# Performance work log

Measured on AMD Instinct MI355X. Metric: run time of the kernel, lower is better.

Reference implementation:

```python
import jax, jax.numpy as jnp
import numpy as np

B, S, D, H, F = 4, 2048, 1024, 16, 4096
DK = D // H
EPS = 1e-5


def layer_norm(x, gamma, beta):
    mu = jnp.mean(x, axis=-1, keepdims=True)
    var = jnp.mean(jnp.square(x - mu), axis=-1, keepdims=True)
    return (x - mu) * jax.lax.rsqrt(var + EPS) * gamma + beta


def setup_inputs() -> dict:
    key = jax.random.key(0)
    ks = jax.random.split(key, 16)
    s = 1.0 / np.sqrt(D)
    sf = 1.0 / np.sqrt(F)
    inp = {
        "x": jax.random.normal(ks[0], (B, S, D), dtype=jnp.float32),
        # causal mask: 0 = blocked, 1 = visible (masked_fill(mask == 0, -1e9))
        "mask": jnp.tril(jnp.ones((S, S), dtype=jnp.int32))[None, None],
        "Wq": jax.random.normal(ks[1], (D, D), dtype=jnp.float32) * s,
        "bq": jnp.zeros((D,), dtype=jnp.float32),
        "Wk": jax.random.normal(ks[2], (D, D), dtype=jnp.float32) * s,
        "bk": jnp.zeros((D,), dtype=jnp.float32),
        "Wv": jax.random.normal(ks[3], (D, D), dtype=jnp.float32) * s,
        "bv": jnp.zeros((D,), dtype=jnp.float32),
        "Wo": jax.random.normal(ks[4], (D, D), dtype=jnp.float32) * s,
        "bo": jnp.zeros((D,), dtype=jnp.float32),
        "g1": jnp.ones((D,), dtype=jnp.float32),
        "b1": jnp.zeros((D,), dtype=jnp.float32),
        "W1": jax.random.normal(ks[5], (D, F), dtype=jnp.float32) * s,
        "c1": jnp.zeros((F,), dtype=jnp.float32),
        "W2": jax.random.normal(ks[6], (F, D), dtype=jnp.float32) * sf,
        "c2": jnp.zeros((D,), dtype=jnp.float32),
        "g2": jnp.ones((D,), dtype=jnp.float32),
        "b2": jnp.zeros((D,), dtype=jnp.float32),
    }
    return inp


def reference(x, mask, Wq, bq, Wk, bk, Wv, bv, Wo, bo, g1, b1, W1, c1, W2, c2, g2, b2):
    b = x.shape[0]
    # qkv projections -> [B, H, S, DK]
    q = (x @ Wq + bq).reshape(b, S, H, DK).transpose(0, 2, 1, 3)
    k = (x @ Wk + bk).reshape(b, S, H, DK).transpose(0, 2, 1, 3)
    v = (x @ Wv + bv).reshape(b, S, H, DK).transpose(0, 2, 1, 3)
    scores = jnp.einsum("bhqd,bhkd->bhqk", q, k) / np.sqrt(DK)
    scores = jnp.where(mask == 0, -1e9, scores)
    attn = jax.nn.softmax(scores, axis=-1)
    out = jnp.einsum("bhqk,bhkd->bhqd", attn, v)
    out = out.transpose(0, 2, 1, 3).reshape(b, S, D)
    attended = out @ Wo + bo
    x = layer_norm(x + attended, g1, b1)
    ff = jax.nn.relu(x @ W1 + c1) @ W2 + c2
    x = layer_norm(x + ff, g2, b2)
    return x
```

## Files before the change

kernel.cpp:

```cpp
#include <hip/hip_runtime.h>
#include <cstdint>
#include <cstddef>

#define DEV __device__ __forceinline__

typedef unsigned short u16;
typedef __attribute__((ext_vector_type(8))) short bf16x8;
typedef __attribute__((ext_vector_type(8))) u16  u16x8;
typedef __attribute__((ext_vector_type(4))) float f32x4;

constexpr int Bn = 4, Sn = 2048, Dn = 1024, Hn = 16, Fn = 4096, DKn = 64;
constexpr int Mn = Bn * Sn;

DEV u16 f2b(float f) {
    unsigned u = __float_as_uint(f);
    unsigned r = (u + 0x7fffu + ((u >> 16) & 1u)) >> 16;
    return (u16)r;
}
DEV float b2f(u16 h) { return __uint_as_float(((unsigned)h) << 16); }

typedef __attribute__((address_space(1))) void gvoid;
typedef __attribute__((address_space(3))) void lvoid;
DEV void gl_lds16(const u16* g, u16* l) {
    __builtin_amdgcn_global_load_lds((gvoid*)g, (lvoid*)l, 16, 0, 0);
}

DEV f32x4 mfma16(bf16x8 a, bf16x8 b, f32x4 c) {
    return __builtin_amdgcn_mfma_f32_16x16x32_bf16(a, b, c, 0, 0, 0);
}

__global__ __launch_bounds__(256) void cvt_f32_bf16(const float* __restrict__ in,
                                                    u16* __restrict__ out) {
    size_t i = ((size_t)blockIdx.x * 256 + threadIdx.x) * 8;
    float4 a = *(const float4*)(in + i);
    float4 b = *(const float4*)(in + i + 4);
    u16x8 o;
    o[0] = f2b(a.x); o[1] = f2b(a.y); o[2] = f2b(a.z); o[3] = f2b(a.w);
    o[4] = f2b(b.x); o[5] = f2b(b.y); o[6] = f2b(b.z); o[7] = f2b(b.w);
    *(u16x8*)(out + i) = o;
}

__global__ __launch_bounds__(256) void transpose_cvt(const float* __restrict__ W,
                                                     u16* __restrict__ Wt, int K, int N) {
    __shared__ float tile[32][33];
    int n0 = blockIdx.x * 32, k0 = blockIdx.y * 32;
    int tx = threadIdx.x, ty = threadIdx.y;
    for (int r = ty; r < 32; r += 8) tile[r][tx] = W[(size_t)(k0 + r) * N + n0 + tx];
    __syncthreads();
    for (int r = ty; r < 32; r += 8) Wt[(size_t)(n0 + r) * K + k0 + tx] = f2b(tile[tx][r]);
}

__global__ __launch_bounds__(256) void vt_kernel(const u16* __restrict__ V,
                                                 u16* __restrict__ Vt) {
    __shared__ u16 t[32][34];
    int s0 = blockIdx.x * 32, d0 = blockIdx.y * 32, bh = blockIdx.z;
    int tx = threadIdx.x, ty = threadIdx.y;
    const u16* in = V + (size_t)bh * Sn * DKn;
    u16* out = Vt + (size_t)bh * DKn * Sn;
    for (int r = ty; r < 32; r += 8) t[r][tx] = in[(size_t)(s0 + r) * DKn + d0 + tx];
    __syncthreads();
    for (int r = ty; r < 32; r += 8) out[(size_t)(d0 + r) * Sn + s0 + tx] = t[tx][r];
}

template <int RELU, int RESID, int OUT_BF16, int QKV>
__global__ __launch_bounds__(256) void gemm_kernel(
    const u16* __restrict__ A, const u16* __restrict__ Bt,
    const float* __restrict__ bias,
    const float* __restrict__ residF, const u16* __restrict__ residB,
    float* __restrict__ Cf, u16* __restrict__ Cb,
    int M, int N, int K, float oscale) {
    constexpr int BK = 32;
    __shared__ __align__(16) u16 As[128 * BK];
    __shared__ __align__(16) u16 Bs[128 * BK];
    const int tid = threadIdx.x, wave = tid >> 6, lane = tid & 63;
    const int quad = lane >> 4, l16 = lane & 15;
    const int row0 = blockIdx.x * 128, col0 = blockIdx.y * 128;
    const int wm = wave & 1, wn = wave >> 1;

    f32x4 acc[4][4];
    for (int mt = 0; mt < 4; mt++)
        for (int nt = 0; nt < 4; nt++)
            acc[mt][nt] = f32x4{0.f, 0.f, 0.f, 0.f};

    const int srow = lane >> 2, scol = (lane & 3) * 8;
    const u16* Ag = A + (size_t)(row0 + wave * 16 + srow) * K + scol;
    const u16* Bg = Bt + (size_t)(col0 + wave * 16 + srow) * K + scol;
    u16* AsW = As + (wave * 16) * BK;
    u16* BsW = Bs + (wave * 16) * BK;

    for (int k0 = 0; k0 < K; k0 += BK) {
        __syncthreads();
        gl_lds16(Ag + k0, AsW);
        gl_lds16(Ag + (size_t)64 * K + k0, AsW + 64 * BK);
        gl_lds16(Bg + k0, BsW);
        gl_lds16(Bg + (size_t)64 * K + k0, BsW + 64 * BK);
        __syncthreads();

        bf16x8 af[4], bfr[4];
        for (int mt = 0; mt < 4; mt++)
            af[mt] = *(const bf16x8*)(As + (wm * 64 + mt * 16 + l16) * BK + quad * 8);
        for (int nt = 0; nt < 4; nt++)
            bfr[nt] = *(const bf16x8*)(Bs + (wn * 64 + nt * 16 + l16) * BK + quad * 8);
        for (int mt = 0; mt < 4; mt++)
            for (int nt = 0; nt < 4; nt++)
                acc[mt][nt] = mfma16(af[mt], bfr[nt], acc[mt][nt]);
    }

    for (int nt = 0; nt < 4; nt++) {
        int col = col0 + wn * 64 + nt * 16 + l16;
        float bv = bias[col];
        for (int mt = 0; mt < 4; mt++) {
            int rbase = row0 + wm * 64 + mt * 16 + quad * 4;
            for (int r = 0; r < 4; r++) {
                int row = rbase + r;
                float v = acc[mt][nt][r] + bv;
                if (RELU) v = fmaxf(v, 0.f);
                if (RESID == 1) v += residF[(size_t)row * N + col];
                if (RESID == 2) v += b2f(residB[(size_t)row * N + col]);
                if (QKV) {
                    int bb = row >> 11, s = row & 2047, h = col >> 6, dk = col & 63;
                    Cb[((size_t)(bb * Hn + h) * Sn + s) * DKn + dk] = f2b(v * oscale);
                } else if (OUT_BF16) {
                    Cb[(size_t)row * N + col] = f2b(v);
                } else {
                    Cf[(size_t)row * N + col] = v;
                }
            }
        }
    }
}

__global__ __launch_bounds__(256, 4) void attn3_kernel(const u16* __restrict__ Q,
                                                       const u16* __restrict__ K,
                                                       const u16* __restrict__ Vt,
                                                       u16* __restrict__ O) {
    constexpr int STR = 72;
    __shared__ __align__(16) u16 Ks[64 * 64];
    __shared__ __align__(16) u16 Vs[64 * 64];
    __shared__ __align__(16) u16 Ps[4][16 * STR];
    int tid = threadIdx.x, wave = tid >> 6, lane = tid & 63;
    int quad = lane >> 4, l16 = lane & 15;
    int bh = blockIdx.y, b = bh >> 4, h = bh & 15;
    int p = blockIdx.x;
    const u16* Qh = Q + (size_t)bh * Sn * DKn;
    const u16* Kh = K + (size_t)bh * Sn * DKn;
    const u16* Vh = Vt + (size_t)bh * DKn * Sn;
    u16* Pw = &Ps[wave][0];

    const int srow = wave * 16 + (lane >> 3);
    const int sblk = lane & 7;
    u16* KsW = Ks + wave * 16 * 64;
    u16* VsW = Vs + wave * 16 * 64;

    for (int t = 0; t < 2; t++) {
        int qt = t ? p : 31 - p;
        int R0 = qt * 64 + wave * 16;

        bf16x8 qf[2];
        for (int h2 = 0; h2 < 2; h2++)
            qf[h2] = *(const bf16x8*)(Qh + (size_t)(R0 + l16) * DKn + h2 * 32 + quad * 8);

        float m_i[4], l_i[4];
        f32x4 accO[4];
        for (int r = 0; r < 4; r++) { m_i[r] = -1e30f; l_i[r] = 0.f; }
        for (int nt = 0; nt < 4; nt++) accO[nt] = f32x4{0.f, 0.f, 0.f, 0.f};

        for (int kt = 0; kt <= qt; kt++) {
            __syncthreads();
            for (int i = 0; i < 2; i++) {
                int r = srow + i * 8;
                int gb = sblk ^ (r & 7);
                gl_lds16(Kh + (size_t)(kt * 64 + r) * DKn + gb * 8, KsW + i * 512);
                gl_lds16(Vh + (size_t)r * Sn + kt * 64 + gb * 8, VsW + i * 512);
            }
            __syncthreads();

            f32x4 sc[4];
            for (int nt = 0; nt < 4; nt++) sc[nt] = f32x4{0.f, 0.f, 0.f, 0.f};
            for (int h2 = 0; h2 < 2; h2++) {
                int bswz = ((h2 * 4 + quad) ^ (l16 & 7)) * 8;
                for (int nt = 0; nt < 4; nt++) {
                    bf16x8 kf = *(const bf16x8*)(Ks + (nt * 16 + l16) * 64 + bswz);
                    sc[nt] = mfma16(qf[h2], kf, sc[nt]);
                }
            }

            if (kt == qt) {
                for (int r = 0; r < 4; r++)
                    for (int nt = 0; nt < 4; nt++)
                        if (nt * 16 + l16 > wave * 16 + quad * 4 + r) sc[nt][r] = -1e30f;
            }

            for (int r = 0; r < 4; r++) {
                float mx = fmaxf(fmaxf(sc[0][r], sc[1][r]), fmaxf(sc[2][r], sc[3][r]));
                for (int off = 1; off < 16; off <<= 1) mx = fmaxf(mx, __shfl_xor(mx, off, 64));
                float mn = fmaxf(m_i[r], mx);
                float al = exp2f(m_i[r] - mn);
                m_i[r] = mn;
                float ps = 0.f;
                for (int nt = 0; nt < 4; nt++) {
                    float pv = exp2f(sc[nt][r] - mn);
                    sc[nt][r] = pv;
                    ps += pv;
                }
                l_i[r] = l_i[r] * al + ps;
                for (int nt = 0; nt < 4; nt++) accO[nt][r] *= al;
            }

            for (int r = 0; r < 4; r++)
                for (int nt = 0; nt < 4; nt++)
                    Pw[(quad * 4 + r) * STR + nt * 16 + l16] = f2b(sc[nt][r]);
            for (int h2 = 0; h2 < 2; h2++) {
                bf16x8 pf = *(const bf16x8*)(Pw + l16 * STR + h2 * 32 + quad * 8);
                int bswz = ((h2 * 4 + quad) ^ (l16 & 7)) * 8;
                for (int nt = 0; nt < 4; nt++) {
                    bf16x8 vf = *(const bf16x8*)(Vs + (nt * 16 + l16) * 64 + bswz);
                    accO[nt] = mfma16(pf, vf, accO[nt]);
                }
            }
        }

        for (int r = 0; r < 4; r++) {
            float lr = l_i[r];
            for (int off = 1; off < 16; off <<= 1) lr += __shfl_xor(lr, off, 64);
            float inv = 1.f / lr;
            int sg = R0 + quad * 4 + r;
            for (int nt = 0; nt < 4; nt++)
                O[((size_t)b * Sn + sg) * Dn + h * DKn + nt * 16 + l16] = f2b(accO[nt][r] * inv);
        }
    }
}

template <int OUT_BF16>
__global__ __launch_bounds__(256) void ln_kernel(const float* __restrict__ in,
                                                 const float* __restrict__ gamma,
                                                 const float* __restrict__ beta,
                                                 float* __restrict__ outF,
                                                 u16* __restrict__ outB) {
    int row = blockIdx.x, tid = threadIdx.x;
    float4 v = ((const float4*)(in + (size_t)row * Dn))[tid];
    float s = v.x + v.y + v.z + v.w;
    float q = v.x * v.x + v.y * v.y + v.z * v.z + v.w * v.w;
    for (int off = 32; off >= 1; off >>= 1) {
        s += __shfl_xor(s, off, 64);
        q += __shfl_xor(q, off, 64);
    }
    __shared__ float rs[4], rq[4];
    int wave = tid >> 6, lane = tid & 63;
    if (lane == 0) { rs[wave] = s; rq[wave] = q; }
    __syncthreads();
    s = rs[0] + rs[1] + rs[2] + rs[3];
    q = rq[0] + rq[1] + rq[2] + rq[3];
    float mu = s * (1.f / Dn);
    float rstd = rsqrtf(q * (1.f / Dn) - mu * mu + 1e-5f);
    float4 g = ((const float4*)gamma)[tid];
    float4 be = ((const float4*)beta)[tid];
    float o0 = (v.x - mu) * rstd * g.x + be.x;
    float o1 = (v.y - mu) * rstd * g.y + be.y;
    float o2 = (v.z - mu) * rstd * g.z + be.z;
    float o3 = (v.w - mu) * rstd * g.w + be.w;
    if (OUT_BF16) {
        ushort4 u;
        u.x = f2b(o0); u.y = f2b(o1); u.z = f2b(o2); u.w = f2b(o3);
        ((ushort4*)outB)[(size_t)row * (Dn / 4) + tid] = u;
    } else {
        ((float4*)outF)[(size_t)row * (Dn / 4) + tid] = make_float4(o0, o1, o2, o3);
    }
}

extern "C" void kernel_launch(void* const* d_in, const int* in_sizes, int n_in,
                              void* d_out, int out_size, void* d_ws, size_t ws_size,
                              hipStream_t stream) {
    const float* x  = (const float*)d_in[0];
    const float* Wq = (const float*)d_in[2];  const float* bq = (const float*)d_in[3];
    const float* Wk = (const float*)d_in[4];  const float* bk = (const float*)d_in[5];
    const float* Wv = (const float*)d_in[6];  const float* bv = (const float*)d_in[7];
    const float* Wo = (const float*)d_in[8];  const float* bo = (const float*)d_in[9];
    const float* g1 = (const float*)d_in[10]; const float* b1 = (const float*)d_in[11];
    const float* W1 = (const float*)d_in[12]; const float* c1 = (const float*)d_in[13];
    const float* W2 = (const float*)d_in[14]; const float* c2 = (const float*)d_in[15];
    const float* g2 = (const float*)d_in[16]; const float* b2 = (const float*)d_in[17];

    char* ws = (char*)d_ws;
    const size_t MB = 1ull << 20;
    u16*   Xb  = (u16*)(ws + 0 * MB);
    u16*   WqT = (u16*)(ws + 16 * MB);
    u16*   WkT = (u16*)(ws + 18 * MB);
    u16*   WvT = (u16*)(ws + 20 * MB);
    u16*   WoT = (u16*)(ws + 22 * MB);
    u16*   W1T = (u16*)(ws + 24 * MB);
    u16*   W2T = (u16*)(ws + 32 * MB);
    u16*   Qb  = (u16*)(ws + 40 * MB);
    u16*   Kb  = (u16*)(ws + 56 * MB);
    u16*   Vb  = (u16*)(ws + 72 * MB);
    u16*   Ob  = (u16*)(ws + 88 * MB);
    u16*   Vt  = (u16*)(ws + 104 * MB);
    float* h1  = (float*)(ws + 104 * MB);
    u16*   ff1 = (u16*)(ws + 136 * MB);
    u16*   ln1b = Qb;
    float* h2   = h1;

    const float qscale = 0.125f * 1.44269504f;

    dim3 tb(32, 8);
    cvt_f32_bf16<<<dim3(Mn * Dn / (256 * 8)), 256, 0, stream>>>(x, Xb);
    transpose_cvt<<<dim3(Dn / 32, Dn / 32), tb, 0, stream>>>(Wq, WqT, Dn, Dn);
    transpose_cvt<<<dim3(Dn / 32, Dn / 32), tb, 0, stream>>>(Wk, WkT, Dn, Dn);
    transpose_cvt<<<dim3(Dn / 32, Dn / 32), tb, 0, stream>>>(Wv, WvT, Dn, Dn);
    transpose_cvt<<<dim3(Dn / 32, Dn / 32), tb, 0, stream>>>(Wo, WoT, Dn, Dn);
    transpose_cvt<<<dim3(Fn / 32, Dn / 32), tb, 0, stream>>>(W1, W1T, Dn, Fn);
    transpose_cvt<<<dim3(Dn / 32, Fn / 32), tb, 0, stream>>>(W2, W2T, Fn, Dn);

    gemm_kernel<0, 0, 1, 1><<<dim3(Mn / 128, Dn / 128), 256, 0, stream>>>(
        Xb, WqT, bq, nullptr, nullptr, nullptr, Qb, Mn, Dn, Dn, qscale);
    gemm_kernel<0, 0, 1, 1><<<dim3(Mn / 128, Dn / 128), 256, 0, stream>>>(
        Xb, WkT, bk, nullptr, nullptr, nullptr, Kb, Mn, Dn, Dn, 1.0f);
    gemm_kernel<0, 0, 1, 1><<<dim3(Mn / 128, Dn / 128), 256, 0, stream>>>(
        Xb, WvT, bv, nullptr, nullptr, nullptr, Vb, Mn, Dn, Dn, 1.0f);

    vt_kernel<<<dim3(Sn / 32, DKn / 32, Bn * Hn), tb, 0, stream>>>(Vb, Vt);

    attn3_kernel<<<dim3(16, Bn * Hn), 256, 0, stream>>>(Qb, Kb, Vt, Ob);

    gemm_kernel<0, 1, 0, 0><<<dim3(Mn / 128, Dn / 128), 256, 0, stream>>>(
        Ob, WoT, bo, x, nullptr, h1, nullptr, Mn, Dn, Dn, 1.0f);
    ln_kernel<1><<<Mn, 256, 0, stream>>>(h1, g1, b1, nullptr, ln1b);

    gemm_kernel<1, 0, 1, 0><<<dim3(Mn / 128, Fn / 128), 256, 0, stream>>>(
        ln1b, W1T, c1, nullptr, nullptr, nullptr, ff1, Mn, Fn, Dn, 1.0f);
    gemm_kernel<0, 2, 0, 0><<<dim3(Mn / 128, Dn / 128), 256, 0, stream>>>(
        ff1, W2T, c2, nullptr, ln1b, h2, nullptr, Mn, Dn, Fn, 1.0f);
    ln_kernel<0><<<Mn, 256, 0, stream>>>(h2, g2, b2, (float*)d_out, nullptr);
}
```

Baseline: 620.7 us.

## Fuse QKV projections into one GEMM and use 128-key attention tiles

The three Q/K/V projection GEMMs become a single launch over N=3*D. Each column block picks its bias and output scale by group and writes to the matching head-major buffer, which cuts launch count and gives a larger grid. The attention kernel now processes 128 keys per iteration instead of 64 and reuses the K shared buffer for the P tile. That halves the number of load/sync rounds per query tile, but needs an extra barrier and wastes half a tile of masked work on even diagonal tiles. The fused GEMM assumes the transposed Q/K/V weights and the Q/K/V output buffers sit contiguously in the workspace.

```diff
diff --git a/kernel.cpp b/kernel.cpp
--- a/kernel.cpp
+++ b/kernel.cpp
@@ -65,7 +65,8 @@
 template <int RELU, int RESID, int OUT_BF16, int QKV>
 __global__ __launch_bounds__(256) void gemm_kernel(
     const u16* __restrict__ A, const u16* __restrict__ Bt,
-    const float* __restrict__ bias,
+    const float* __restrict__ bias, const float* __restrict__ biasB,
+    const float* __restrict__ biasC,
     const float* __restrict__ residF, const u16* __restrict__ residB,
     float* __restrict__ Cf, u16* __restrict__ Cb,
     int M, int N, int K, float oscale) {
@@ -106,9 +107,17 @@
                 acc[mt][nt] = mfma16(af[mt], bfr[nt], acc[mt][nt]);
     }
 
+    int g = 0; const float* bp = bias; float osc = 1.0f;
+    if (QKV == 2) {
+        g = (col0 >> 10);
+        bp = (g == 0) ? bias : ((g == 1) ? biasB : biasC);
+        osc = (g == 0) ? oscale : 1.0f;
+    }
+
     for (int nt = 0; nt < 4; nt++) {
         int col = col0 + wn * 64 + nt * 16 + l16;
-        float bv = bias[col];
+        int cc = col & 1023;
+        float bv = (QKV == 2) ? bp[cc] : bias[col];
         for (int mt = 0; mt < 4; mt++) {
             int rbase = row0 + wm * 64 + mt * 16 + quad * 4;
             for (int r = 0; r < 4; r++) {
@@ -117,9 +126,10 @@
                 if (RELU) v = fmaxf(v, 0.f);
                 if (RESID == 1) v += residF[(size_t)row * N + col];
                 if (RESID == 2) v += b2f(residB[(size_t)row * N + col]);
-                if (QKV) {
-                    int bb = row >> 11, s = row & 2047, h = col >> 6, dk = col & 63;
-                    Cb[((size_t)(bb * Hn + h) * Sn + s) * DKn + dk] = f2b(v * oscale);
+                if (QKV == 2) {
+                    int bb = row >> 11, s = row & 2047, h = cc >> 6, dk = cc & 63;
+                    Cb[(size_t)g * Mn * Dn +
+                       ((size_t)(bb * Hn + h) * Sn + s) * DKn + dk] = f2b(v * osc);
                 } else if (OUT_BF16) {
                     Cb[(size_t)row * N + col] = f2b(v);
                 } else {
@@ -130,14 +140,12 @@
     }
 }
 
-__global__ __launch_bounds__(256, 4) void attn3_kernel(const u16* __restrict__ Q,
+__global__ __launch_bounds__(256, 4) void attn4_kernel(const u16* __restrict__ Q,
                                                        const u16* __restrict__ K,
                                                        const u16* __restrict__ Vt,
                                                        u16* __restrict__ O) {
-    constexpr int STR = 72;
-    __shared__ __align__(16) u16 Ks[64 * 64];
-    __shared__ __align__(16) u16 Vs[64 * 64];
-    __shared__ __align__(16) u16 Ps[4][16 * STR];
+    __shared__ __align__(16) u16 Ks[128 * 64];
+    __shared__ __align__(16) u16 Vs[64 * 128];
     int tid = threadIdx.x, wave = tid >> 6, lane = tid & 63;
     int quad = lane >> 4, l16 = lane & 15;
     int bh = blockIdx.y, b = bh >> 4, h = bh & 15;
@@ -145,12 +153,10 @@
     const u16* Qh = Q + (size_t)bh * Sn * DKn;
     const u16* Kh = K + (size_t)bh * Sn * DKn;
     const u16* Vh = Vt + (size_t)bh * DKn * Sn;
-    u16* Pw = &Ps[wave][0];
-
-    const int srow = wave * 16 + (lane >> 3);
-    const int sblk = lane & 7;
-    u16* KsW = Ks + wave * 16 * 64;
-    u16* VsW = Vs + wave * 16 * 64;
+    u16* Pw = Ks + wave * 16 * 128;
+
+    const int ksr = wave * 32 + (lane >> 3), ksb = lane & 7;
+    const int vsr = wave * 16 + (lane >> 4), vsb = lane & 15;
 
     for (int t = 0; t < 2; t++) {
         int qt = t ? p : 31 - p;
@@ -165,40 +171,45 @@
         for (int r = 0; r < 4; r++) { m_i[r] = -1e30f; l_i[r] = 0.f; }
         for (int nt = 0; nt < 4; nt++) accO[nt] = f32x4{0.f, 0.f, 0.f, 0.f};
 
-        for (int kt = 0; kt <= qt; kt++) {
+        int n2 = (qt + 2) >> 1;
+        for (int kt2 = 0; kt2 < n2; kt2++) {
             __syncthreads();
-            for (int i = 0; i < 2; i++) {
-                int r = srow + i * 8;
-                int gb = sblk ^ (r & 7);
-                gl_lds16(Kh + (size_t)(kt * 64 + r) * DKn + gb * 8, KsW + i * 512);
-                gl_lds16(Vh + (size_t)r * Sn + kt * 64 + gb * 8, VsW + i * 512);
+            for (int i = 0; i < 4; i++) {
+                int rk = ksr + i * 8;
+                gl_lds16(Kh + (size_t)(kt2 * 128 + rk) * DKn + ((ksb ^ (rk & 7)) * 8),
+                         Ks + (wave * 32 + i * 8) * 64);
+                int rv = vsr + i * 4;
+                gl_lds16(Vh + (size_t)rv * Sn + kt2 * 128 + ((vsb ^ (rv & 7)) * 8),
+                         Vs + (wave * 16 + i * 4) * 128);
             }
             __syncthreads();
 
-            f32x4 sc[4];
-            for (int nt = 0; nt < 4; nt++) sc[nt] = f32x4{0.f, 0.f, 0.f, 0.f};
-            for (int h2 = 0; h2 < 2; h2++) {
-                int bswz = ((h2 * 4 + quad) ^ (l16 & 7)) * 8;
-                for (int nt = 0; nt < 4; nt++) {
-                    bf16x8 kf = *(const bf16x8*)(Ks + (nt * 16 + l16) * 64 + bswz);
+            f32x4 sc[8];
+            for (int nt = 0; nt < 8; nt++) sc[nt] = f32x4{0.f, 0.f, 0.f, 0.f};
+            for (int h2 = 0; h2 < 2; h2++)
+                for (int nt = 0; nt < 8; nt++) {
+                    bf16x8 kf = *(const bf16x8*)(Ks + (nt * 16 + l16) * 64 +
+                                                 (((h2 * 4 + quad) ^ (l16 & 7)) * 8));
                     sc[nt] = mfma16(qf[h2], kf, sc[nt]);
                 }
-            }
-
-            if (kt == qt) {
+            __syncthreads();
+
+            if (kt2 == n2 - 1) {
+                int crow = R0 + quad * 4 - kt2 * 128;
                 for (int r = 0; r < 4; r++)
-                    for (int nt = 0; nt < 4; nt++)
-                        if (nt * 16 + l16 > wave * 16 + quad * 4 + r) sc[nt][r] = -1e30f;
+                    for (int nt = 0; nt < 8; nt++)
+                        if (nt * 16 + l16 > crow + r) sc[nt][r] = -1e30f;
             }
 
             for (int r = 0; r < 4; r++) {
-                float mx = fmaxf(fmaxf(sc[0][r], sc[1][r]), fmaxf(sc[2][r], sc[3][r]));
+                float mx = sc[0][r];
+                for (int nt = 1; nt < 8; nt++) mx = fmaxf(mx, sc[nt][r]);
                 for (int off = 1; off < 16; off <<= 1) mx = fmaxf(mx, __shfl_xor(mx, off, 64));
                 float mn = fmaxf(m_i[r], mx);
                 float al = exp2f(m_i[r] - mn);
                 m_i[r] = mn;
                 float ps = 0.f;
-                for (int nt = 0; nt < 4; nt++) {
+                for (int nt = 0; nt < 8; nt++) {
                     float pv = exp2f(sc[nt][r] - mn);
                     sc[nt][r] = pv;
                     ps += pv;
@@ -208,13 +219,13 @@
             }
 
             for (int r = 0; r < 4; r++)
-                for (int nt = 0; nt < 4; nt++)
-                    Pw[(quad * 4 + r) * STR + nt * 16 + l16] = f2b(sc[nt][r]);
-            for (int h2 = 0; h2 < 2; h2++) {
-                bf16x8 pf = *(const bf16x8*)(Pw + l16 * STR + h2 * 32 + quad * 8);
-                int bswz = ((h2 * 4 + quad) ^ (l16 & 7)) * 8;
+                for (int nt = 0; nt < 8; nt++)
+                    Pw[(quad * 4 + r) * 128 + nt * 16 + l16] = f2b(sc[nt][r]);
+            for (int c = 0; c < 4; c++) {
+                bf16x8 pf = *(const bf16x8*)(Pw + l16 * 128 + c * 32 + quad * 8);
                 for (int nt = 0; nt < 4; nt++) {
-                    bf16x8 vf = *(const bf16x8*)(Vs + (nt * 16 + l16) * 64 + bswz);
+                    bf16x8 vf = *(const bf16x8*)(Vs + (nt * 16 + l16) * 128 +
+                                                 (((c * 4 + quad) ^ (l16 & 7)) * 8));
                     accO[nt] = mfma16(pf, vf, accO[nt]);
                 }
             }
@@ -311,24 +322,20 @@
     transpose_cvt<<<dim3(Fn / 32, Dn / 32), tb, 0, stream>>>(W1, W1T, Dn, Fn);
     transpose_cvt<<<dim3(Dn / 32, Fn / 32), tb, 0, stream>>>(W2, W2T, Fn, Dn);
 
-    gemm_kernel<0, 0, 1, 1><<<dim3(Mn / 128, Dn / 128), 256, 0, stream>>>(
-        Xb, WqT, bq, nullptr, nullptr, nullptr, Qb, Mn, Dn, Dn, qscale);
-    gemm_kernel<0, 0, 1, 1><<<dim3(Mn / 128, Dn / 128), 256, 0, stream>>>(
-        Xb, WkT, bk, nullptr, nullptr, nullptr, Kb, Mn, Dn, Dn, 1.0f);
-    gemm_kernel<0, 0, 1, 1><<<dim3(Mn / 128, Dn / 128), 256, 0, stream>>>(
-        Xb, WvT, bv, nullptr, nullptr, nullptr, Vb, Mn, Dn, Dn, 1.0f);
+    gemm_kernel<0, 0, 1, 2><<<dim3(Mn / 128, 3 * Dn / 128), 256, 0, stream>>>(
+        Xb, WqT, bq, bk, bv, nullptr, nullptr, nullptr, Qb, Mn, 3 * Dn, Dn, qscale);
 
     vt_kernel<<<dim3(Sn / 32, DKn / 32, Bn * Hn), tb, 0, stream>>>(Vb, Vt);
 
-    attn3_kernel<<<dim3(16, Bn * Hn), 256, 0, stream>>>(Qb, Kb, Vt, Ob);
+    attn4_kernel<<<dim3(16, Bn * Hn), 256, 0, stream>>>(Qb, Kb, Vt, Ob);
 
     gemm_kernel<0, 1, 0, 0><<<dim3(Mn / 128, Dn / 128), 256, 0, stream>>>(
-        Ob, WoT, bo, x, nullptr, h1, nullptr, Mn, Dn, Dn, 1.0f);
+        Ob, WoT, bo, nullptr, nullptr, x, nullptr, h1, nullptr, Mn, Dn, Dn, 1.0f);
     ln_kernel<1><<<Mn, 256, 0, stream>>>(h1, g1, b1, nullptr, ln1b);
 
     gemm_kernel<1, 0, 1, 0><<<dim3(Mn / 128, Fn / 128), 256, 0, stream>>>(
-        ln1b, W1T, c1, nullptr, nullptr, nullptr, ff1, Mn, Fn, Dn, 1.0f);
+        ln1b, W1T, c1, nullptr, nullptr, nullptr, nullptr, nullptr, ff1, Mn, Fn, Dn, 1.0f);
     gemm_kernel<0, 2, 0, 0><<<dim3(Mn / 128, Dn / 128), 256, 0, stream>>>(
-        ff1, W2T, c2, nullptr, ln1b, h2, nullptr, Mn, Dn, Fn, 1.0f);
+        ff1, W2T, c2, nullptr, nullptr, nullptr, ln1b, h2, nullptr, Mn, Dn, Fn, 1.0f);
     ln_kernel<0><<<Mn, 256, 0, stream>>>(h2, g2, b2, (float*)d_out, nullptr);
 }
```

Result: faster. 608.0 us (-2.0%).
